# Kernel optimization log

Hardware: AMD Instinct MI355X
Metric: run time of the kernel (lower is better)

The kernel has to match this reference:

```python
import jax, jax.numpy as jnp
import numpy as np

D_MODEL = 1024
N_HEADS = 16
HEAD_DIM = D_MODEL // N_HEADS
ROPE_BASE = 10000.0
RMS_EPS = 1e-5


def setup_inputs() -> dict:
    key = jax.random.key(0)
    k1, k2, k3 = jax.random.split(key, 3)
    B, T = 2, 2048
    x = jax.random.normal(k1, (B, T, D_MODEL), dtype=jnp.float32)
    norm_w = jnp.ones((D_MODEL,), dtype=jnp.float32)
    w_qkv = jax.random.normal(k2, (3 * D_MODEL, D_MODEL), dtype=jnp.float32) * (D_MODEL ** -0.5)
    w_out = jax.random.normal(k3, (D_MODEL, D_MODEL), dtype=jnp.float32) * (D_MODEL ** -0.5)
    return {"x": x, "norm_w": norm_w, "w_qkv": w_qkv, "w_out": w_out}


def _rope_cos_sin(T, dtype):
    inv_freq = 1.0 / (ROPE_BASE ** (jnp.arange(0, HEAD_DIM, 2, dtype=jnp.float32) / HEAD_DIM))
    t = jnp.arange(T, dtype=jnp.float32)
    freqs = t[:, None] * inv_freq[None, :]            # [T, HEAD_DIM//2]
    emb = jnp.concatenate([freqs, freqs], axis=-1)    # [T, HEAD_DIM]
    return jnp.cos(emb).astype(dtype), jnp.sin(emb).astype(dtype)


def _rotate_half(x):
    x1, x2 = jnp.split(x, 2, axis=-1)
    return jnp.concatenate([-x2, x1], axis=-1)


def reference(x, norm_w, w_qkv, w_out):
    B, T, _ = x.shape
    residual = x
    # RMSNorm
    rms = jax.lax.rsqrt(jnp.mean(x * x, axis=-1, keepdims=True) + RMS_EPS)
    xn = x * rms * norm_w
    # QKV projection (torch Linear: x @ W.T)
    qkv = xn @ w_qkv.T                                  # [B, T, 3*D]
    qkv = qkv.reshape(B, T, 3, N_HEADS, HEAD_DIM)
    q, k, v = qkv[:, :, 0], qkv[:, :, 1], qkv[:, :, 2]  # [B, T, H, hd]
    # RoPE on q, k
    cos, sin = _rope_cos_sin(T, q.dtype)                # [T, hd]
    cos = cos[None, :, None, :]
    sin = sin[None, :, None, :]
    q = q * cos + _rotate_half(q) * sin
    k = k * cos + _rotate_half(k) * sin
    # Bidirectional SDPA: [B, H, T, hd]
    qh = q.transpose(0, 2, 1, 3)
    kh = k.transpose(0, 2, 1, 3)
    vh = v.transpose(0, 2, 1, 3)
    scale = HEAD_DIM ** -0.5
    scores = jnp.einsum('bhqd,bhkd->bhqk', qh, kh) * scale
    attn = jax.nn.softmax(scores, axis=-1)
    out = jnp.einsum('bhqk,bhkd->bhqd', attn, vh)       # [B, H, T, hd]
    out = out.transpose(0, 2, 1, 3).reshape(B, T, D_MODEL)
    out = out @ w_out.T
    return residual + out
```

## Files before the change

kernel.cpp:

```cpp
#include <hip/hip_runtime.h>
#include <hip/hip_bf16.h>
#include <math.h>


typedef __bf16 bf16;
typedef __bf16 bf16x8 __attribute__((ext_vector_type(8)));
typedef __bf16 bf16x4 __attribute__((ext_vector_type(4)));
typedef float  f32x4  __attribute__((ext_vector_type(4)));

#define GLOAD16(g, l) __builtin_amdgcn_global_load_lds( \
    (const __attribute__((address_space(1))) void*)(g),  \
    (__attribute__((address_space(3))) void*)(l), 16, 0, 0)

__device__ __forceinline__ unsigned pk2(float a, float b) {
  unsigned short lo = __builtin_bit_cast(unsigned short, (bf16)a);
  unsigned short hi = __builtin_bit_cast(unsigned short, (bf16)b);
  return (unsigned)lo | ((unsigned)hi << 16);
}

__global__ __launch_bounds__(256) void k_cvt(const float* __restrict__ src,
    bf16* __restrict__ dst, int n) {
  int i = (blockIdx.x * 256 + threadIdx.x) * 8;
  if (i >= n) return;
  float4 a = *(const float4*)(src + i);
  float4 b = *(const float4*)(src + i + 4);
  bf16x8 o;
  o[0] = (bf16)a.x; o[1] = (bf16)a.y; o[2] = (bf16)a.z; o[3] = (bf16)a.w;
  o[4] = (bf16)b.x; o[5] = (bf16)b.y; o[6] = (bf16)b.z; o[7] = (bf16)b.w;
  *(bf16x8*)(dst + i) = o;
}

__global__ __launch_bounds__(256) void k_rmsnorm(const float* __restrict__ x,
    const float* __restrict__ w, bf16* __restrict__ xn) {
  const int row = blockIdx.x, tid = threadIdx.x;
  float4 v = *(const float4*)(x + (size_t)row * 1024 + tid * 4);
  float ss = v.x * v.x + v.y * v.y + v.z * v.z + v.w * v.w;
  for (int m = 32; m >= 1; m >>= 1) ss += __shfl_xor(ss, m);
  __shared__ float red[4];
  if ((tid & 63) == 0) red[tid >> 6] = ss;
  __syncthreads();
  float ms = (red[0] + red[1] + red[2] + red[3]) * (1.f / 1024.f);
  float r = rsqrtf(ms + 1e-5f);
  float4 wv = *(const float4*)(w + tid * 4);
  bf16x4 o;
  o[0] = (bf16)(v.x * r * wv.x); o[1] = (bf16)(v.y * r * wv.y);
  o[2] = (bf16)(v.z * r * wv.z); o[3] = (bf16)(v.w * r * wv.w);
  *(bf16x4*)(xn + (size_t)row * 1024 + tid * 4) = o;
}

template<int RESID>
__global__ __launch_bounds__(256, 2) void k_gemm_bt(const bf16* __restrict__ A,
    const bf16* __restrict__ B, const float* __restrict__ R, void* __restrict__ Cv,
    int M, int N, int K, int lda) {
  const int tid = threadIdx.x;
  const int lane = tid & 63, L15 = lane & 15, quad = lane >> 4;
  const int wave = tid >> 6, wr = wave >> 1, wc = wave & 1;
  const int n0 = blockIdx.x * 128, m0 = blockIdx.y * 128;
  __shared__ __align__(16) bf16 smem[17408];
  bf16* sA = smem; bf16* sB = smem + 8192;
  f32x4 acc[4][4];
  const f32x4 z = {0.f, 0.f, 0.f, 0.f};
  for (int i = 0; i < 4; i++) for (int j = 0; j < 4; j++) acc[i][j] = z;

  for (int k0 = 0; k0 < K; k0 += 64) {
    const bf16* Ab = A + (size_t)m0 * lda + k0;
    const bf16* Bb = B + (size_t)n0 * K + k0;
    for (int p = 0; p < 4; p++) {
      int s = p * 256 + tid, r = s >> 3, c8 = (s & 7) ^ (r & 7);
      GLOAD16(Ab + (size_t)r * lda + c8 * 8, sA + s * 8);
      GLOAD16(Bb + (size_t)r * K + c8 * 8, sB + s * 8);
    }
    __syncthreads();
    for (int kk = 0; kk < 2; kk++) {
      bf16x8 af[4], bfv[4];
      for (int i = 0; i < 4; i++) {
        int ra = wr * 64 + i * 16 + L15;
        af[i] = *(const bf16x8*)(sA + ra * 64 + (((kk * 4 + quad) ^ (ra & 7)) * 8));
        int rb = wc * 64 + i * 16 + L15;
        bfv[i] = *(const bf16x8*)(sB + rb * 64 + (((kk * 4 + quad) ^ (rb & 7)) * 8));
      }
      for (int mt = 0; mt < 4; mt++)
        for (int nt = 0; nt < 4; nt++)
          acc[mt][nt] = __builtin_amdgcn_mfma_f32_16x16x32_bf16(af[mt], bfv[nt], acc[mt][nt], 0, 0, 0);
    }
    __syncthreads();
  }
  bf16* sC = smem;
  for (int mt = 0; mt < 4; mt++) for (int nt = 0; nt < 4; nt++) {
    int r = wr * 64 + mt * 16 + quad * 4, c = wc * 64 + nt * 16 + L15;
    f32x4 v = acc[mt][nt];
    for (int g = 0; g < 4; g++) sC[(r + g) * 136 + c] = (bf16)v[g];
  }
  __syncthreads();
  const int rr = tid >> 1, sg = (tid & 1) * 64;
  const size_t row = (size_t)m0 + rr;
  const bf16* src = sC + rr * 136 + sg;
  if (RESID) {
    float* Cf = (float*)Cv;
    const float* rs = R + row * N + n0 + sg;
    float* dst = Cf + row * N + n0 + sg;
    for (int i = 0; i < 16; i++) {
      bf16x4 u = *(const bf16x4*)(src + i * 4);
      float4 rv = *(const float4*)(rs + i * 4);
      float4 o;
      o.x = (float)u[0] + rv.x; o.y = (float)u[1] + rv.y;
      o.z = (float)u[2] + rv.z; o.w = (float)u[3] + rv.w;
      *(float4*)(dst + i * 4) = o;
    }
  } else {
    bf16* Cb = (bf16*)Cv;
    bf16* dst = Cb + row * N + n0 + sg;
    for (int i = 0; i < 8; i++)
      *(bf16x8*)(dst + i * 8) = *(const bf16x8*)(src + i * 8);
  }
}

__global__ __launch_bounds__(256) void k_rope(bf16* __restrict__ qkv,
    bf16* __restrict__ vt) {
  const int blk = blockIdx.x;
  const int tt = blk & 31, h = (blk >> 5) & 15, b = blk >> 9;
  const int tid = threadIdx.x;
  const int bh = b * 16 + h;
  {
    const int tl = tid >> 2, dp = (tid & 3) * 8;
    const int tg = tt * 64 + tl;
    bf16* base = qkv + (size_t)(b * 2048 + tg) * 3072 + h * 64;
    bf16x8 qlo = *(const bf16x8*)(base + dp);
    bf16x8 qhi = *(const bf16x8*)(base + dp + 32);
    bf16x8 klo = *(const bf16x8*)(base + 1024 + dp);
    bf16x8 khi = *(const bf16x8*)(base + 1024 + dp + 32);
    bf16x8 oql, oqh, okl, okh;
    for (int j = 0; j < 8; j++) {
      float invf = exp2f(-0.41524101186f * (float)(dp + j));
      float th = (float)tg * invf;
      float sn, cs;
      sincosf(th, &sn, &cs);
      float a0 = (float)qlo[j], a1 = (float)qhi[j];
      float b0 = (float)klo[j], b1 = (float)khi[j];
      oql[j] = (bf16)(a0 * cs - a1 * sn);
      oqh[j] = (bf16)(a1 * cs + a0 * sn);
      okl[j] = (bf16)(b0 * cs - b1 * sn);
      okh[j] = (bf16)(b1 * cs + b0 * sn);
    }
    *(bf16x8*)(base + dp) = oql; *(bf16x8*)(base + dp + 32) = oqh;
    *(bf16x8*)(base + 1024 + dp) = okl; *(bf16x8*)(base + 1024 + dp + 32) = okh;
  }
  __shared__ __align__(16) bf16 sT[64 * 72];
  for (int p = 0; p < 2; p++) {
    int s = p * 256 + tid, tl = s >> 3, c = s & 7;
    const bf16* vsrc = qkv + (size_t)(b * 2048 + tt * 64 + tl) * 3072 + 2048 + h * 64 + c * 8;
    *(bf16x8*)(sT + tl * 72 + c * 8) = *(const bf16x8*)vsrc;
  }
  __syncthreads();
  for (int p = 0; p < 2; p++) {
    int s = p * 256 + tid, d = s >> 3, tc = s & 7;
    bf16x8 v;
    for (int j = 0; j < 8; j++) v[j] = sT[(tc * 8 + j) * 72 + d];
    *(bf16x8*)(vt + (size_t)bh * 131072 + (size_t)d * 2048 + tt * 64 + tc * 8) = v;
  }
}

__global__ __launch_bounds__(256, 2) void k_attn(bf16* __restrict__ qkv,
    const bf16* __restrict__ vt) {
  const int tid = threadIdx.x;
  const int lane = tid & 63, L15 = lane & 15, quad = lane >> 4;
  const int wave = tid >> 6;
  const int bh = blockIdx.y, b = bh >> 4, h = bh & 15;
  const int q0 = blockIdx.x * 128;
  const bf16* Q  = qkv + (size_t)b * 2048 * 3072 + h * 64;
  const bf16* Kg = qkv + (size_t)b * 2048 * 3072 + 1024 + h * 64;
  const bf16* Vg = vt + (size_t)bh * 131072;
  __shared__ __align__(16) bf16 sK[8192];
  __shared__ __align__(16) bf16 sV[8192];
  __shared__ __align__(16) bf16 sP[17408];

  bf16x8 qf[2][2];
  for (int qt = 0; qt < 2; qt++) for (int kk = 0; kk < 2; kk++) {
    int rq = q0 + wave * 32 + qt * 16 + L15;
    qf[qt][kk] = *(const bf16x8*)(Q + (size_t)rq * 3072 + kk * 32 + quad * 8);
  }
  f32x4 o[4][2];
  const f32x4 z = {0.f, 0.f, 0.f, 0.f};
  for (int i = 0; i < 4; i++) for (int j = 0; j < 2; j++) o[i][j] = z;
  float mrun[2] = {-1e30f, -1e30f};
  float lrun[2] = {0.f, 0.f};
  const float c2 = 0.125f;

  for (int kv0 = 0; kv0 < 2048; kv0 += 128) {
    __syncthreads();
    const bf16* Kb = Kg + (size_t)kv0 * 3072;
    for (int p = 0; p < 4; p++) {
      int s = p * 256 + tid, r = s >> 3, c8 = (s & 7) ^ (r & 7);
      GLOAD16(Kb + (size_t)r * 3072 + c8 * 8, sK + s * 8);
    }
    for (int p = 0; p < 4; p++) {
      int s = p * 256 + tid, r = s >> 4, cl = s & 15;
      int c8 = (cl & 8) | ((cl ^ (r & 7)) & 7);
      GLOAD16(Vg + (size_t)r * 2048 + kv0 + c8 * 8, sV + s * 8);
    }
    __syncthreads();
    f32x4 st[8][2];
    for (int i = 0; i < 8; i++) for (int j = 0; j < 2; j++) st[i][j] = z;
    for (int kk = 0; kk < 2; kk++) {
      bf16x8 kf[8];
      for (int kvt = 0; kvt < 8; kvt++) {
        int rk = kvt * 16 + L15;
        kf[kvt] = *(const bf16x8*)(sK + rk * 64 + (((kk * 4 + quad) ^ (rk & 7)) * 8));
      }
      for (int kvt = 0; kvt < 8; kvt++)
        for (int qt = 0; qt < 2; qt++)
          st[kvt][qt] = __builtin_amdgcn_mfma_f32_16x16x32_bf16(kf[kvt], qf[qt][kk], st[kvt][qt], 0, 0, 0);
    }
    for (int qt = 0; qt < 2; qt++) {
      float m = st[0][qt][0];
      for (int kvt = 0; kvt < 8; kvt++)
        for (int g = 0; g < 4; g++) m = fmaxf(m, st[kvt][qt][g]);
      m = fmaxf(m, __shfl_xor(m, 16));
      m = fmaxf(m, __shfl_xor(m, 32));
      float mnew = fmaxf(mrun[qt], m);
      float alpha = __expf((mrun[qt] - mnew) * c2);
      float mc = mnew * c2;
      float ls = 0.f;
      int rq = wave * 32 + qt * 16 + L15;
      for (int kvt = 0; kvt < 8; kvt++) {
        float p0 = __expf(st[kvt][qt][0] * c2 - mc);
        float p1 = __expf(st[kvt][qt][1] * c2 - mc);
        float p2 = __expf(st[kvt][qt][2] * c2 - mc);
        float p3 = __expf(st[kvt][qt][3] * c2 - mc);
        ls += (p0 + p1) + (p2 + p3);
        uint2 w2; w2.x = pk2(p0, p1); w2.y = pk2(p2, p3);
        *(uint2*)(sP + rq * 136 + kvt * 16 + quad * 4) = w2;
      }
      ls += __shfl_xor(ls, 16);
      ls += __shfl_xor(ls, 32);
      lrun[qt] = lrun[qt] * alpha + ls;
      mrun[qt] = mnew;
      for (int dt = 0; dt < 4; dt++) o[dt][qt] *= alpha;
    }
    for (int kc = 0; kc < 4; kc++) {
      bf16x8 vf[4], pf[2];
      for (int dt = 0; dt < 4; dt++) {
        int rd = dt * 16 + L15;
        int c = kc * 4 + quad;
        int cs = (c & 8) | ((c ^ (rd & 7)) & 7);
        vf[dt] = *(const bf16x8*)(sV + rd * 128 + cs * 8);
      }
      for (int qt = 0; qt < 2; qt++) {
        int rq = wave * 32 + qt * 16 + L15;
        pf[qt] = *(const bf16x8*)(sP + rq * 136 + kc * 32 + quad * 8);
      }
      for (int dt = 0; dt < 4; dt++)
        for (int qt = 0; qt < 2; qt++)
          o[dt][qt] = __builtin_amdgcn_mfma_f32_16x16x32_bf16(vf[dt], pf[qt], o[dt][qt], 0, 0, 0);
    }
  }
  float invl[2] = {1.f / lrun[0], 1.f / lrun[1]};
  __syncthreads();
  bf16* sO = sP;
  for (int dt = 0; dt < 4; dt++) for (int qt = 0; qt < 2; qt++) {
    f32x4 v = o[dt][qt] * invl[qt];
    int ql = wave * 32 + qt * 16 + L15;
    uint2 w2; w2.x = pk2(v[0], v[1]); w2.y = pk2(v[2], v[3]);
    *(uint2*)(sO + ql * 72 + dt * 16 + quad * 4) = w2;
  }
  __syncthreads();
  const int rr = tid >> 1, sg = (tid & 1) * 32;
  const bf16* src = sO + rr * 72 + sg;
  bf16* dst = qkv + (size_t)(b * 2048 + q0 + rr) * 3072 + h * 64 + sg;
  for (int i = 0; i < 4; i++)
    *(bf16x8*)(dst + i * 8) = *(const bf16x8*)(src + i * 8);
}

extern "C" void kernel_launch(void* const* d_in, const int* in_sizes, int n_in,
                              void* d_out, int out_size, void* d_ws, size_t ws_size,
                              hipStream_t stream) {
  (void)in_sizes; (void)n_in; (void)out_size;
  const float* x     = (const float*)d_in[0];
  const float* normw = (const float*)d_in[1];
  const float* wqkv  = (const float*)d_in[2];
  const float* wout  = (const float*)d_in[3];
  float* out = (float*)d_out;
  bf16* ws  = (bf16*)d_ws;
  const size_t NQKV = (size_t)4096 * 3072, NXN = (size_t)4096 * 1024;
  const size_t NWQ = (size_t)3072 * 1024, NWO = (size_t)1024 * 1024;
  const size_t need = (NQKV + NXN + NWQ + NWO) * sizeof(bf16);
  if (ws_size < need) return;
  bf16* qkv    = ws;
  bf16* xn     = qkv + NQKV;
  bf16* vtp    = xn;
  bf16* wqkvb  = xn + NXN;
  bf16* woutb  = wqkvb + NWQ;
  k_cvt<<<(int)(NWQ / 8 / 256), 256, 0, stream>>>(wqkv, wqkvb, (int)NWQ);
  k_cvt<<<(int)(NWO / 8 / 256), 256, 0, stream>>>(wout, woutb, (int)NWO);
  k_rmsnorm<<<4096, 256, 0, stream>>>(x, normw, xn);
  k_gemm_bt<0><<<dim3(24, 32), 256, 0, stream>>>(xn, wqkvb, nullptr, qkv, 4096, 3072, 1024, 1024);
  k_rope<<<1024, 256, 0, stream>>>(qkv, vtp);
  k_attn<<<dim3(16, 32), 256, 0, stream>>>(qkv, vtp);
  k_gemm_bt<1><<<dim3(8, 32), 256, 0, stream>>>(qkv, woutb, x, out, 4096, 1024, 1024, 3072);
}
```

Measured before the change: 222.0 us.

## Halve attention query tile, keep P in registers via lane shuffles

The attention kernel now processes 64 queries per block instead of 128, doubling the grid and raising the launch-bounds occupancy hint to 4 blocks per CU. The softmax probabilities are packed in registers and redistributed with cross-lane shuffles for the PV MFMA, so the shared-memory P buffer and its round trip are removed. Softmax switches to exp2 with a folded log2e scale, and one block barrier in the epilogue is dropped. The trade-off is that each K/V tile loaded into LDS is reused by half as many queries, which doubles K/V load traffic per unit of work.

```diff
diff --git a/kernel.cpp b/kernel.cpp
--- a/kernel.cpp
+++ b/kernel.cpp
@@ -7,6 +7,7 @@
 typedef __bf16 bf16x8 __attribute__((ext_vector_type(8)));
 typedef __bf16 bf16x4 __attribute__((ext_vector_type(4)));
 typedef float  f32x4  __attribute__((ext_vector_type(4)));
+typedef unsigned long long u64x2 __attribute__((ext_vector_type(2)));
 
 #define GLOAD16(g, l) __builtin_amdgcn_global_load_lds( \
     (const __attribute__((address_space(1))) void*)(g),  \
@@ -160,31 +161,34 @@
   }
 }
 
-__global__ __launch_bounds__(256, 2) void k_attn(bf16* __restrict__ qkv,
+__global__ __launch_bounds__(256, 4) void k_attn(bf16* __restrict__ qkv,
     const bf16* __restrict__ vt) {
   const int tid = threadIdx.x;
   const int lane = tid & 63, L15 = lane & 15, quad = lane >> 4;
   const int wave = tid >> 6;
   const int bh = blockIdx.y, b = bh >> 4, h = bh & 15;
-  const int q0 = blockIdx.x * 128;
+  const int q0 = blockIdx.x * 64;
   const bf16* Q  = qkv + (size_t)b * 2048 * 3072 + h * 64;
   const bf16* Kg = qkv + (size_t)b * 2048 * 3072 + 1024 + h * 64;
   const bf16* Vg = vt + (size_t)bh * 131072;
   __shared__ __align__(16) bf16 sK[8192];
   __shared__ __align__(16) bf16 sV[8192];
-  __shared__ __align__(16) bf16 sP[17408];
-
-  bf16x8 qf[2][2];
-  for (int qt = 0; qt < 2; qt++) for (int kk = 0; kk < 2; kk++) {
-    int rq = q0 + wave * 32 + qt * 16 + L15;
-    qf[qt][kk] = *(const bf16x8*)(Q + (size_t)rq * 3072 + kk * 32 + quad * 8);
-  }
-  f32x4 o[4][2];
+
+  bf16x8 qf[2];
+  {
+    int rq = q0 + wave * 16 + L15;
+    qf[0] = *(const bf16x8*)(Q + (size_t)rq * 3072 + quad * 8);
+    qf[1] = *(const bf16x8*)(Q + (size_t)rq * 3072 + 32 + quad * 8);
+  }
+  f32x4 o[4];
   const f32x4 z = {0.f, 0.f, 0.f, 0.f};
-  for (int i = 0; i < 4; i++) for (int j = 0; j < 2; j++) o[i][j] = z;
-  float mrun[2] = {-1e30f, -1e30f};
-  float lrun[2] = {0.f, 0.f};
-  const float c2 = 0.125f;
+  for (int i = 0; i < 4; i++) o[i] = z;
+  float mrun = -1e30f;
+  float lrun = 0.f;
+  const float SC = 0.125f * 1.44269504f;
+  const int srcA = (quad & 1) * 32 + L15;
+  const int srcB = srcA + 16;
+  const bool hi_reg = ((quad >> 1) & 1) != 0;
 
   for (int kv0 = 0; kv0 < 2048; kv0 += 128) {
     __syncthreads();
@@ -199,8 +203,8 @@
       GLOAD16(Vg + (size_t)r * 2048 + kv0 + c8 * 8, sV + s * 8);
     }
     __syncthreads();
-    f32x4 st[8][2];
-    for (int i = 0; i < 8; i++) for (int j = 0; j < 2; j++) st[i][j] = z;
+    f32x4 st[8];
+    for (int i = 0; i < 8; i++) st[i] = z;
     for (int kk = 0; kk < 2; kk++) {
       bf16x8 kf[8];
       for (int kvt = 0; kvt < 8; kvt++) {
@@ -208,67 +212,67 @@
         kf[kvt] = *(const bf16x8*)(sK + rk * 64 + (((kk * 4 + quad) ^ (rk & 7)) * 8));
       }
       for (int kvt = 0; kvt < 8; kvt++)
-        for (int qt = 0; qt < 2; qt++)
-          st[kvt][qt] = __builtin_amdgcn_mfma_f32_16x16x32_bf16(kf[kvt], qf[qt][kk], st[kvt][qt], 0, 0, 0);
-    }
-    for (int qt = 0; qt < 2; qt++) {
-      float m = st[0][qt][0];
-      for (int kvt = 0; kvt < 8; kvt++)
-        for (int g = 0; g < 4; g++) m = fmaxf(m, st[kvt][qt][g]);
-      m = fmaxf(m, __shfl_xor(m, 16));
-      m = fmaxf(m, __shfl_xor(m, 32));
-      float mnew = fmaxf(mrun[qt], m);
-      float alpha = __expf((mrun[qt] - mnew) * c2);
-      float mc = mnew * c2;
-      float ls = 0.f;
-      int rq = wave * 32 + qt * 16 + L15;
-      for (int kvt = 0; kvt < 8; kvt++) {
-        float p0 = __expf(st[kvt][qt][0] * c2 - mc);
-        float p1 = __expf(st[kvt][qt][1] * c2 - mc);
-        float p2 = __expf(st[kvt][qt][2] * c2 - mc);
-        float p3 = __expf(st[kvt][qt][3] * c2 - mc);
-        ls += (p0 + p1) + (p2 + p3);
-        uint2 w2; w2.x = pk2(p0, p1); w2.y = pk2(p2, p3);
-        *(uint2*)(sP + rq * 136 + kvt * 16 + quad * 4) = w2;
-      }
-      ls += __shfl_xor(ls, 16);
-      ls += __shfl_xor(ls, 32);
-      lrun[qt] = lrun[qt] * alpha + ls;
-      mrun[qt] = mnew;
-      for (int dt = 0; dt < 4; dt++) o[dt][qt] *= alpha;
-    }
+        st[kvt] = __builtin_amdgcn_mfma_f32_16x16x32_bf16(kf[kvt], qf[kk], st[kvt], 0, 0, 0);
+    }
+    float m = st[0][0];
+    for (int kvt = 0; kvt < 8; kvt++)
+      for (int g = 0; g < 4; g++) m = fmaxf(m, st[kvt][g]);
+    m = fmaxf(m, __shfl_xor(m, 16));
+    m = fmaxf(m, __shfl_xor(m, 32));
+    float mnew = fmaxf(mrun, m * SC);
+    float alpha = exp2f(mrun - mnew);
+    float ls = 0.f;
+    u64x2 pk[4];
+    for (int kvt = 0; kvt < 8; kvt++) {
+      float p0 = exp2f(st[kvt][0] * SC - mnew);
+      float p1 = exp2f(st[kvt][1] * SC - mnew);
+      float p2 = exp2f(st[kvt][2] * SC - mnew);
+      float p3 = exp2f(st[kvt][3] * SC - mnew);
+      ls += (p0 + p1) + (p2 + p3);
+      unsigned long long w = (unsigned long long)pk2(p0, p1) |
+                             ((unsigned long long)pk2(p2, p3) << 32);
+      pk[kvt >> 1][kvt & 1] = w;
+    }
+    ls += __shfl_xor(ls, 16);
+    ls += __shfl_xor(ls, 32);
+    lrun = lrun * alpha + ls;
+    mrun = mnew;
+    for (int dt = 0; dt < 4; dt++) o[dt] *= alpha;
     for (int kc = 0; kc < 4; kc++) {
-      bf16x8 vf[4], pf[2];
+      bf16x8 vf[4];
       for (int dt = 0; dt < 4; dt++) {
         int rd = dt * 16 + L15;
         int c = kc * 4 + quad;
         int cs = (c & 8) | ((c ^ (rd & 7)) & 7);
         vf[dt] = *(const bf16x8*)(sV + rd * 128 + cs * 8);
       }
-      for (int qt = 0; qt < 2; qt++) {
-        int rq = wave * 32 + qt * 16 + L15;
-        pf[qt] = *(const bf16x8*)(sP + rq * 136 + kc * 32 + quad * 8);
-      }
+      unsigned long long ev = pk[kc][0], ov = pk[kc][1];
+      unsigned long long loE = __shfl(ev, srcA, 64);
+      unsigned long long loO = __shfl(ov, srcA, 64);
+      unsigned long long hiE = __shfl(ev, srcB, 64);
+      unsigned long long hiO = __shfl(ov, srcB, 64);
+      u64x2 t;
+      t[0] = hi_reg ? loO : loE;
+      t[1] = hi_reg ? hiO : hiE;
+      bf16x8 pf = __builtin_bit_cast(bf16x8, t);
       for (int dt = 0; dt < 4; dt++)
-        for (int qt = 0; qt < 2; qt++)
-          o[dt][qt] = __builtin_amdgcn_mfma_f32_16x16x32_bf16(vf[dt], pf[qt], o[dt][qt], 0, 0, 0);
-    }
-  }
-  float invl[2] = {1.f / lrun[0], 1.f / lrun[1]};
+        o[dt] = __builtin_amdgcn_mfma_f32_16x16x32_bf16(vf[dt], pf, o[dt], 0, 0, 0);
+    }
+  }
+  float invl = 1.f / lrun;
   __syncthreads();
-  bf16* sO = sP;
-  for (int dt = 0; dt < 4; dt++) for (int qt = 0; qt < 2; qt++) {
-    f32x4 v = o[dt][qt] * invl[qt];
-    int ql = wave * 32 + qt * 16 + L15;
+  bf16* sO = sK;
+  for (int dt = 0; dt < 4; dt++) {
+    f32x4 v = o[dt] * invl;
+    int ql = wave * 16 + L15;
     uint2 w2; w2.x = pk2(v[0], v[1]); w2.y = pk2(v[2], v[3]);
     *(uint2*)(sO + ql * 72 + dt * 16 + quad * 4) = w2;
   }
-  __syncthreads();
-  const int rr = tid >> 1, sg = (tid & 1) * 32;
+  const int rr = tid >> 2, sg = (tid & 3) * 16;
   const bf16* src = sO + rr * 72 + sg;
   bf16* dst = qkv + (size_t)(b * 2048 + q0 + rr) * 3072 + h * 64 + sg;
-  for (int i = 0; i < 4; i++)
-    *(bf16x8*)(dst + i * 8) = *(const bf16x8*)(src + i * 8);
+  *(bf16x8*)(dst) = *(const bf16x8*)(src);
+  *(bf16x8*)(dst + 8) = *(const bf16x8*)(src + 8);
 }
 
 extern "C" void kernel_launch(void* const* d_in, const int* in_sizes, int n_in,
@@ -295,6 +299,6 @@
   k_rmsnorm<<<4096, 256, 0, stream>>>(x, normw, xn);
   k_gemm_bt<0><<<dim3(24, 32), 256, 0, stream>>>(xn, wqkvb, nullptr, qkv, 4096, 3072, 1024, 1024);
   k_rope<<<1024, 256, 0, stream>>>(qkv, vtp);
-  k_attn<<<dim3(16, 32), 256, 0, stream>>>(qkv, vtp);
+  k_attn<<<dim3(32, 32), 256, 0, stream>>>(qkv, vtp);
   k_gemm_bt<1><<<dim3(8, 32), 256, 0, stream>>>(qkv, woutb, x, out, 4096, 1024, 1024, 3072);
 }
```

Measured after the change: 256.1 us. +15.4%, slower.
